# Optimization experiments

Hardware: AMD Instinct MI355X
Metric: run time of the kernel (lower is better)

The kernel has to match this reference:

```python
import jax, jax.numpy as jnp
import numpy as np

K = 32
START = K - 2  # index of <START>
STOP = K - 1   # index of <STOP>
NEG = -10000.0
B, T = 512, 2048


def setup_inputs() -> dict:
    key = jax.random.key(0)
    k1, k2, k3, k4 = jax.random.split(key, 4)
    feats = jax.random.normal(k1, (B, T, K), dtype=jnp.float32)
    transitions = jax.random.normal(k2, (K, K), dtype=jnp.float32)
    # constraints set in __init__: never transition TO START, never FROM STOP
    transitions = transitions.at[START, :].set(NEG).at[:, STOP].set(NEG)
    tags = jax.random.randint(k3, (B, T), 0, K - 2)          # real tags only
    lens = jnp.maximum(jax.random.randint(k4, (B,), 0, T), 1)  # at least 1 token
    return {"feats": feats, "transitions": transitions, "tags": tags, "lens": lens}


def _crf_loss(feats, transitions, tags, lens):
    Bn, Tn, Kn = feats.shape
    # ---- forward algorithm (log-partition) ----
    init = jnp.full((Bn, Kn), NEG, feats.dtype).at[:, START].set(0.0)

    def step(alpha, emit):
        # alpha[b,prev] + trans[next,prev] -> logsumexp over prev, then + emit[b,next]
        nxt = jax.scipy.special.logsumexp(
            alpha[:, None, :] + transitions[None, :, :], axis=2) + emit
        return nxt, nxt

    _, alphas = jax.lax.scan(step, init, jnp.swapaxes(feats, 0, 1))  # [T,B,K]
    alphas = jnp.concatenate([init[None], alphas], axis=0)           # [T+1,B,K]
    alpha_at_len = alphas[lens, jnp.arange(Bn)]                      # [B,K]
    forward_score = jax.scipy.special.logsumexp(
        alpha_at_len + transitions[STOP][None, :], axis=1)           # [B]

    # ---- gold score ----
    tags_stop = jnp.where(jnp.arange(Tn)[None, :] < lens[:, None], tags, STOP)
    pad_start = jnp.concatenate(
        [jnp.full((Bn, 1), START, tags.dtype), tags], axis=1)        # [B,T+1]
    pad_stop = jnp.concatenate(
        [tags_stop, jnp.full((Bn, 1), STOP, tags.dtype)], axis=1)    # [B,T+1]
    trans_mask = jnp.arange(Tn + 1)[None, :] <= lens[:, None]        # len+1 transitions
    trans_sc = jnp.where(trans_mask, transitions[pad_stop, pad_start], 0.0).sum(axis=1)
    emit_mask = jnp.arange(Tn)[None, :] < lens[:, None]
    emit_sc = jnp.where(
        emit_mask,
        jnp.take_along_axis(feats, tags[:, :, None], axis=2)[..., 0],
        0.0).sum(axis=1)
    gold_score = trans_sc + emit_sc

    return jnp.mean(forward_score - gold_score)


def reference(feats, transitions, tags, lens):
    return _crf_loss(feats, transitions, tags, lens)
```

## Files before the change

### kernel.cpp

```cpp
#include <hip/hip_runtime.h>
#include <cstdint>
#include <cstddef>

#define Kn 32
#define Bn 512
#define Tn 2048
#define CH 128
#define NC (Tn / CH)
#define GP 4
#define MMB (Bn * 2)
#define GB  Bn
#define START 30
#define STOP 31
#define LN2F 0.69314718055994530942f

typedef __attribute__((ext_vector_type(8))) short bf16x8;
typedef __attribute__((ext_vector_type(16))) float f32x16;
typedef __attribute__((ext_vector_type(2))) float f32x2;

union BF8 { bf16x8 v; unsigned u[4]; };

__device__ __forceinline__ unsigned pk2z(float lo, float hi) {
  return __builtin_amdgcn_perm(__float_as_uint(hi), __float_as_uint(lo),
                               0x07060302u);
}

__device__ __forceinline__ float bcast32(float v, int idx) {
  return __shfl(v, idx, 32);
}

__device__ __forceinline__ void plswap(unsigned& a, unsigned& b) {
  asm("v_permlane32_swap_b32 %0, %1" : "+v"(a), "+v"(b));
}

struct Chain {
  unsigned bu[8];
  f32x16 acc;
  float off;
  float ring[8];
  const float* fb;
  int lim;
};

__global__ __launch_bounds__(256, 3) void crf_fused(
    const float* __restrict__ feats, const float* __restrict__ trans,
    const int* __restrict__ tags, const int* __restrict__ lens,
    float* __restrict__ pmats, float* __restrict__ poffs,
    float* __restrict__ gold_part) {
  const int wid = threadIdx.x >> 6;
  const int lane = threadIdx.x & 63;

  if (blockIdx.x < MMB) {
    const int b = blockIdx.x >> 1;
    const int widx = (blockIdx.x & 1) * 4 + wid;
    const int len = lens[b];
    const int c0 = 2 * widx, c1 = c0 + 1;
    const int n0 = min(max(len - c0 * CH, 0), CH);
    const int n1 = min(max(len - c1 * CH, 0), CH);
    if (n0 == 0) return;

    const int m = lane & 31;
    const int h = lane >> 5;

    f32x2 e1[4], e2[4];
    {
      const float* tr = trans + m * Kn + 8 * h;
#pragma unroll
      for (int j = 0; j < 4; ++j) {
        e1[j] = (f32x2){__expf(tr[2 * j]) * 0.0078125f,
                        __expf(tr[2 * j + 1]) * 0.0078125f};
        e2[j] = (f32x2){__expf(tr[16 + 2 * j]) * 0.0078125f,
                        __expf(tr[16 + 2 * j + 1]) * 0.0078125f};
      }
    }
    const f32x16 zf = {0.f, 0.f, 0.f, 0.f, 0.f, 0.f, 0.f, 0.f,
                       0.f, 0.f, 0.f, 0.f, 0.f, 0.f, 0.f, 0.f};

    auto init_chain = [&](Chain& ch, int c) {
      unsigned i1[4] = {0, 0, 0, 0}, i2[4] = {0, 0, 0, 0};
      int j = m - 8 * h;
      if (0 <= j && j < 8) i1[j >> 1] = (j & 1) ? 0x3F800000u : 0x00003F80u;
      j = m - 16 - 8 * h;
      if (0 <= j && j < 8) i2[j >> 1] = (j & 1) ? 0x3F800000u : 0x00003F80u;
#pragma unroll
      for (int k = 0; k < 4; ++k) { ch.bu[k] = i1[k]; ch.bu[4 + k] = i2[k]; }
      ch.off = 0.f;
      const int t0 = c * CH;
      ch.fb = feats + ((size_t)b * Tn + t0) * Kn + m;
      ch.lim = Tn - 1 - t0;
#pragma unroll
      for (int i = 0; i < 8; ++i) ch.ring[i] = ch.fb[(size_t)min(i, ch.lim) * Kn];
    };

    auto mm = [&](Chain& ch, float f, bool rn) {
      const float w = __expf(f);
      const f32x2 w2 = {w, w};
      BF8 A1, A2, B1, B2;
#pragma unroll
      for (int j = 0; j < 4; ++j) {
        const f32x2 p1 = e1[j] * w2;
        const f32x2 p2 = e2[j] * w2;
        A1.u[j] = pk2z(p1.x, p1.y);
        A2.u[j] = pk2z(p2.x, p2.y);
        B1.u[j] = ch.bu[j];
        B2.u[j] = ch.bu[4 + j];
      }
      f32x16 acc = __builtin_amdgcn_mfma_f32_32x32x16_bf16(A2.v, B2.v, zf, 0, 0, 0);
      acc = __builtin_amdgcn_mfma_f32_32x32x16_bf16(A1.v, B1.v, acc, 0, 0, 0);

      if (rn) {
        float mx = acc[0];
#pragma unroll
        for (int r = 1; r < 16; ++r) mx = fmaxf(mx, acc[r]);
#pragma unroll
        for (int d = 1; d < 64; d <<= 1) mx = fmaxf(mx, __shfl_xor(mx, d));
        const int e = (int)((__float_as_uint(mx) >> 23) & 255u);
        const float sc = __uint_as_float((unsigned)(254 - e) << 23);
#pragma unroll
        for (int r = 0; r < 16; ++r) acc[r] *= sc;
        ch.off += (float)(e - 127) * LN2F;
      }

      unsigned qa = pk2z(acc[0], acc[1]);
      unsigned qb = pk2z(acc[2], acc[3]);
      unsigned qc = pk2z(acc[4], acc[5]);
      unsigned qd = pk2z(acc[6], acc[7]);
      unsigned qe = pk2z(acc[8], acc[9]);
      unsigned qf = pk2z(acc[10], acc[11]);
      unsigned qg = pk2z(acc[12], acc[13]);
      unsigned qh = pk2z(acc[14], acc[15]);
      plswap(qa, qc);
      plswap(qb, qd);
      plswap(qe, qg);
      plswap(qf, qh);
      ch.bu[0] = qa; ch.bu[1] = qb; ch.bu[2] = qc; ch.bu[3] = qd;
      ch.bu[4] = qe; ch.bu[5] = qf; ch.bu[6] = qg; ch.bu[7] = qh;
      ch.acc = acc;
    };

    Chain ch0, ch1;
    init_chain(ch0, c0);
    if (n1) init_chain(ch1, c1);

    const int nb0 = n0 >> 3;
    const int nb1 = n1 >> 3;
    int t = 0;
    for (int mb = 0; mb < nb1; ++mb) {
#pragma unroll
      for (int i = 0; i < 8; ++i) {
        const float f0 = ch0.ring[i];
        ch0.ring[i] = ch0.fb[(size_t)min(t + i + 8, ch0.lim) * Kn];
        const float f1 = ch1.ring[i];
        ch1.ring[i] = ch1.fb[(size_t)min(t + i + 8, ch1.lim) * Kn];
        const bool rn = ((t + i) & 31) == 31;
        mm(ch0, f0, rn);
        mm(ch1, f1, rn);
      }
      t += 8;
    }
    for (int mb = nb1; mb < nb0; ++mb) {
#pragma unroll
      for (int i = 0; i < 8; ++i) {
        const float f0 = ch0.ring[i];
        ch0.ring[i] = ch0.fb[(size_t)min(t + i + 8, ch0.lim) * Kn];
        mm(ch0, f0, ((t + i) & 31) == 31);
      }
      t += 8;
    }
    const int r0 = n0 & 7;
    for (int i = 0; i < r0; ++i) mm(ch0, ch0.ring[i], false);
    const int r1 = n1 & 7;
    for (int i = 0; i < r1; ++i) mm(ch1, ch1.ring[i], false);

    {
      float* pm = pmats + (size_t)(b * NC + c0) * (Kn * Kn);
#pragma unroll
      for (int r = 0; r < 16; ++r) {
        const int row = (r & 3) + 8 * (r >> 2) + 4 * h;
        pm[row * Kn + m] = ch0.acc[r];
      }
      if (lane == 0) poffs[b * NC + c0] = ch0.off + 7.0f * LN2F * (float)n0;
    }
    if (n1) {
      float* pm = pmats + (size_t)(b * NC + c1) * (Kn * Kn);
#pragma unroll
      for (int r = 0; r < 16; ++r) {
        const int row = (r & 3) + 8 * (r >> 2) + 4 * h;
        pm[row * Kn + m] = ch1.acc[r];
      }
      if (lane == 0) poffs[b * NC + c1] = ch1.off + 7.0f * LN2F * (float)n1;
    }
  } else {
    const int b = blockIdx.x - MMB;
    const int len = lens[b];
    const int* tg = tags + (size_t)b * Tn;
    const float* fbp = feats + (size_t)b * Tn * Kn;
    float acc = 0.f;
    for (int tt = 64 * wid + lane; tt < len; tt += 256) {
      const int tag = tg[tt];
      const int prev = tt ? tg[tt - 1] : START;
      acc += fbp[(size_t)tt * Kn + tag] + trans[tag * Kn + prev];
      if (tt == len - 1) acc += trans[STOP * Kn + tag];
    }
#pragma unroll
    for (int msk = 32; msk >= 1; msk >>= 1) acc += __shfl_xor(acc, msk);
    if (lane == 0) gold_part[b * GP + wid] = acc;
  }
}

__device__ __forceinline__ float renorm_s(float& s, float off) {
  int e = (int)((__float_as_uint(s) >> 23) & 255u);
  e = max(e, __shfl_xor(e, 1));
  e = max(e, __shfl_xor(e, 2));
  e = max(e, __shfl_xor(e, 4));
  e = max(e, __shfl_xor(e, 8));
  e = max(e, __shfl_xor(e, 16));
  s *= __uint_as_float((unsigned)(254 - e) << 23);
  return off + (float)(e - 127) * LN2F;
}

__global__ __launch_bounds__(256, 2) void crf_apply(
    const float* __restrict__ trans, const int* __restrict__ lens,
    const float* __restrict__ pmats, const float* __restrict__ poffs,
    const float* __restrict__ gold_part, float* __restrict__ out) {
  __shared__ float4 smat[NC * 256];
  const int tid = threadIdx.x;
  const int b = blockIdx.x;
  const int len = lens[b];
  const int nc = (len + CH - 1) / CH;

  const float4* gp = (const float4*)(pmats + (size_t)b * NC * (Kn * Kn));
  for (int qq = tid; qq < nc * 256; qq += 256) {
    const int row = (qq >> 3) & 31;
    const int g = qq & 7;
    smat[(qq & ~7) | (g ^ (row & 7))] = gp[qq];
  }
  __syncthreads();
  if (tid >= 64) return;

  const int lane = tid;
  const int n = lane & 31;
  const int hb = (lane >> 5) * 16;
  const int g0 = hb >> 2;
  const int nsw = n & 7;
  float s = (n == START) ? 1.0f : 0.0f;
  float off = 0.0f;
  for (int c = 0; c < nc; ++c) {
    const float4* mr = &smat[(c << 8) | (n << 3)];
    const float4 p0 = mr[(g0 + 0) ^ nsw];
    const float4 p1 = mr[(g0 + 1) ^ nsw];
    const float4 p2 = mr[(g0 + 2) ^ nsw];
    const float4 p3 = mr[(g0 + 3) ^ nsw];
    float a0 = 0.f, a1 = 0.f, a2 = 0.f, a3 = 0.f;
    a0 = fmaf(bcast32(s, hb + 0), p0.x, a0);
    a0 = fmaf(bcast32(s, hb + 1), p0.y, a0);
    a0 = fmaf(bcast32(s, hb + 2), p0.z, a0);
    a0 = fmaf(bcast32(s, hb + 3), p0.w, a0);
    a1 = fmaf(bcast32(s, hb + 4), p1.x, a1);
    a1 = fmaf(bcast32(s, hb + 5), p1.y, a1);
    a1 = fmaf(bcast32(s, hb + 6), p1.z, a1);
    a1 = fmaf(bcast32(s, hb + 7), p1.w, a1);
    a2 = fmaf(bcast32(s, hb + 8), p2.x, a2);
    a2 = fmaf(bcast32(s, hb + 9), p2.y, a2);
    a2 = fmaf(bcast32(s, hb + 10), p2.z, a2);
    a2 = fmaf(bcast32(s, hb + 11), p2.w, a2);
    a3 = fmaf(bcast32(s, hb + 12), p3.x, a3);
    a3 = fmaf(bcast32(s, hb + 13), p3.y, a3);
    a3 = fmaf(bcast32(s, hb + 14), p3.z, a3);
    a3 = fmaf(bcast32(s, hb + 15), p3.w, a3);
    float p = (a0 + a1) + (a2 + a3);
    p += __shfl_xor(p, 32);
    s = p;
    off = renorm_s(s, off);
    off += poffs[b * NC + c];
  }
  const float es = __expf(trans[STOP * Kn + n]);
  float q = s * es;
#pragma unroll
  for (int d = 1; d < 32; d <<= 1) q += __shfl_xor(q, d);
  if (lane == 0) {
    const float fs = __logf(q) + off;
    float gs = 0.f;
#pragma unroll
    for (int gi = 0; gi < GP; ++gi) gs += gold_part[b * GP + gi];
    atomicAdd(out, (fs - gs) * (1.0f / (float)Bn));
  }
}

extern "C" void kernel_launch(void* const* d_in, const int* in_sizes, int n_in,
                              void* d_out, int out_size, void* d_ws, size_t ws_size,
                              hipStream_t stream) {
  const float* feats = (const float*)d_in[0];
  const float* trans = (const float*)d_in[1];
  const int* tags = (const int*)d_in[2];
  const int* lens = (const int*)d_in[3];

  float* gold_part = (float*)d_ws;
  float* poffs = gold_part + (size_t)Bn * GP;
  float* pmats = poffs + (size_t)Bn * NC;

  hipMemsetAsync(d_out, 0, (size_t)out_size * sizeof(float), stream);
  crf_fused<<<MMB + GB, 256, 0, stream>>>(feats, trans, tags, lens, pmats,
                                          poffs, gold_part);
  crf_apply<<<Bn, 256, 0, stream>>>(trans, lens, pmats, poffs, gold_part,
                                    (float*)d_out);
}
```

Before: 286.0 us.

## Use one chunk per wave with LDS double-buffered feature staging

Each wave now processes a single 128-step chunk instead of interleaving two independent chains, and the grid grows from two to four blocks per batch row. Feature rows are loaded from global memory as coalesced float4 loads into a per-wave double-buffered LDS staging area 32 timesteps deep, replacing strided scalar global loads. The next quarter is prefetched while the current one is computed. Occupancy hint rises from 3 to 4 blocks per CU. Dropping the second chain removes the instruction-level parallelism that hid MFMA latency across two dependent recurrences, which may expose the serial dependency chain.

```diff
diff --git a/kernel.cpp b/kernel.cpp
--- a/kernel.cpp
+++ b/kernel.cpp
@@ -8,11 +8,13 @@
 #define CH 128
 #define NC (Tn / CH)
 #define GP 4
-#define MMB (Bn * 2)
+#define MMB (Bn * (NC / 4))
 #define GB  Bn
 #define START 30
 #define STOP 31
 #define LN2F 0.69314718055994530942f
+#define QS 32
+#define QF (QS * Kn)
 
 typedef __attribute__((ext_vector_type(8))) short bf16x8;
 typedef __attribute__((ext_vector_type(16))) float f32x16;
@@ -33,31 +35,21 @@
   asm("v_permlane32_swap_b32 %0, %1" : "+v"(a), "+v"(b));
 }
 
-struct Chain {
-  unsigned bu[8];
-  f32x16 acc;
-  float off;
-  float ring[8];
-  const float* fb;
-  int lim;
-};
-
-__global__ __launch_bounds__(256, 3) void crf_fused(
+__global__ __launch_bounds__(256, 4) void crf_fused(
     const float* __restrict__ feats, const float* __restrict__ trans,
     const int* __restrict__ tags, const int* __restrict__ lens,
     float* __restrict__ pmats, float* __restrict__ poffs,
     float* __restrict__ gold_part) {
+  __shared__ float lds[4][2][QF];
   const int wid = threadIdx.x >> 6;
   const int lane = threadIdx.x & 63;
 
   if (blockIdx.x < MMB) {
-    const int b = blockIdx.x >> 1;
-    const int widx = (blockIdx.x & 1) * 4 + wid;
+    const int b = blockIdx.x >> 2;
+    const int c = (blockIdx.x & 3) * 4 + wid;
     const int len = lens[b];
-    const int c0 = 2 * widx, c1 = c0 + 1;
-    const int n0 = min(max(len - c0 * CH, 0), CH);
-    const int n1 = min(max(len - c1 * CH, 0), CH);
-    if (n0 == 0) return;
+    const int nsteps = min(max(len - c * CH, 0), CH);
+    if (nsteps == 0) return;
 
     const int m = lane & 31;
     const int h = lane >> 5;
@@ -73,26 +65,24 @@
                         __expf(tr[16 + 2 * j + 1]) * 0.0078125f};
       }
     }
+    unsigned bu[8];
+    {
+      const int j1 = m - 8 * h;
+      const int j2 = m - 16 - 8 * h;
+#pragma unroll
+      for (int k = 0; k < 4; ++k) {
+        bu[k] = (j1 == 2 * k) ? 0x00003F80u
+                              : (j1 == 2 * k + 1) ? 0x3F800000u : 0u;
+        bu[4 + k] = (j2 == 2 * k) ? 0x00003F80u
+                                  : (j2 == 2 * k + 1) ? 0x3F800000u : 0u;
+      }
+    }
     const f32x16 zf = {0.f, 0.f, 0.f, 0.f, 0.f, 0.f, 0.f, 0.f,
                        0.f, 0.f, 0.f, 0.f, 0.f, 0.f, 0.f, 0.f};
-
-    auto init_chain = [&](Chain& ch, int c) {
-      unsigned i1[4] = {0, 0, 0, 0}, i2[4] = {0, 0, 0, 0};
-      int j = m - 8 * h;
-      if (0 <= j && j < 8) i1[j >> 1] = (j & 1) ? 0x3F800000u : 0x00003F80u;
-      j = m - 16 - 8 * h;
-      if (0 <= j && j < 8) i2[j >> 1] = (j & 1) ? 0x3F800000u : 0x00003F80u;
-#pragma unroll
-      for (int k = 0; k < 4; ++k) { ch.bu[k] = i1[k]; ch.bu[4 + k] = i2[k]; }
-      ch.off = 0.f;
-      const int t0 = c * CH;
-      ch.fb = feats + ((size_t)b * Tn + t0) * Kn + m;
-      ch.lim = Tn - 1 - t0;
-#pragma unroll
-      for (int i = 0; i < 8; ++i) ch.ring[i] = ch.fb[(size_t)min(i, ch.lim) * Kn];
-    };
-
-    auto mm = [&](Chain& ch, float f, bool rn) {
+    f32x16 acc;
+    float off = 0.0f;
+
+    auto mmstep = [&](float f, bool rn) {
       const float w = __expf(f);
       const f32x2 w2 = {w, w};
       BF8 A1, A2, B1, B2;
@@ -102,10 +92,10 @@
         const f32x2 p2 = e2[j] * w2;
         A1.u[j] = pk2z(p1.x, p1.y);
         A2.u[j] = pk2z(p2.x, p2.y);
-        B1.u[j] = ch.bu[j];
-        B2.u[j] = ch.bu[4 + j];
-      }
-      f32x16 acc = __builtin_amdgcn_mfma_f32_32x32x16_bf16(A2.v, B2.v, zf, 0, 0, 0);
+        B1.u[j] = bu[j];
+        B2.u[j] = bu[4 + j];
+      }
+      acc = __builtin_amdgcn_mfma_f32_32x32x16_bf16(A2.v, B2.v, zf, 0, 0, 0);
       acc = __builtin_amdgcn_mfma_f32_32x32x16_bf16(A1.v, B1.v, acc, 0, 0, 0);
 
       if (rn) {
@@ -118,7 +108,7 @@
         const float sc = __uint_as_float((unsigned)(254 - e) << 23);
 #pragma unroll
         for (int r = 0; r < 16; ++r) acc[r] *= sc;
-        ch.off += (float)(e - 127) * LN2F;
+        off += (float)(e - 127) * LN2F;
       }
 
       unsigned qa = pk2z(acc[0], acc[1]);
@@ -133,63 +123,74 @@
       plswap(qb, qd);
       plswap(qe, qg);
       plswap(qf, qh);
-      ch.bu[0] = qa; ch.bu[1] = qb; ch.bu[2] = qc; ch.bu[3] = qd;
-      ch.bu[4] = qe; ch.bu[5] = qf; ch.bu[6] = qg; ch.bu[7] = qh;
-      ch.acc = acc;
+      bu[0] = qa; bu[1] = qb; bu[2] = qc; bu[3] = qd;
+      bu[4] = qe; bu[5] = qf; bu[6] = qg; bu[7] = qh;
     };
 
-    Chain ch0, ch1;
-    init_chain(ch0, c0);
-    if (n1) init_chain(ch1, c1);
-
-    const int nb0 = n0 >> 3;
-    const int nb1 = n1 >> 3;
-    int t = 0;
-    for (int mb = 0; mb < nb1; ++mb) {
-#pragma unroll
-      for (int i = 0; i < 8; ++i) {
-        const float f0 = ch0.ring[i];
-        ch0.ring[i] = ch0.fb[(size_t)min(t + i + 8, ch0.lim) * Kn];
-        const float f1 = ch1.ring[i];
-        ch1.ring[i] = ch1.fb[(size_t)min(t + i + 8, ch1.lim) * Kn];
-        const bool rn = ((t + i) & 31) == 31;
-        mm(ch0, f0, rn);
-        mm(ch1, f1, rn);
-      }
-      t += 8;
-    }
-    for (int mb = nb1; mb < nb0; ++mb) {
-#pragma unroll
-      for (int i = 0; i < 8; ++i) {
-        const float f0 = ch0.ring[i];
-        ch0.ring[i] = ch0.fb[(size_t)min(t + i + 8, ch0.lim) * Kn];
-        mm(ch0, f0, ((t + i) & 31) == 31);
-      }
-      t += 8;
-    }
-    const int r0 = n0 & 7;
-    for (int i = 0; i < r0; ++i) mm(ch0, ch0.ring[i], false);
-    const int r1 = n1 & 7;
-    for (int i = 0; i < r1; ++i) mm(ch1, ch1.ring[i], false);
+    const float* gsrc = feats + ((size_t)b * Tn + (size_t)c * CH) * Kn;
+    float* myl = &lds[wid][0][0];
 
     {
-      float* pm = pmats + (size_t)(b * NC + c0) * (Kn * Kn);
-#pragma unroll
-      for (int r = 0; r < 16; ++r) {
-        const int row = (r & 3) + 8 * (r >> 2) + 4 * h;
-        pm[row * Kn + m] = ch0.acc[r];
-      }
-      if (lane == 0) poffs[b * NC + c0] = ch0.off + 7.0f * LN2F * (float)n0;
-    }
-    if (n1) {
-      float* pm = pmats + (size_t)(b * NC + c1) * (Kn * Kn);
-#pragma unroll
-      for (int r = 0; r < 16; ++r) {
-        const int row = (r & 3) + 8 * (r >> 2) + 4 * h;
-        pm[row * Kn + m] = ch1.acc[r];
-      }
-      if (lane == 0) poffs[b * NC + c1] = ch1.off + 7.0f * LN2F * (float)n1;
-    }
+      float4 v0 = *(const float4*)(gsrc + 0 * 256 + lane * 4);
+      float4 v1 = *(const float4*)(gsrc + 1 * 256 + lane * 4);
+      float4 v2 = *(const float4*)(gsrc + 2 * 256 + lane * 4);
+      float4 v3 = *(const float4*)(gsrc + 3 * 256 + lane * 4);
+      *(float4*)(myl + 0 * 256 + lane * 4) = v0;
+      *(float4*)(myl + 1 * 256 + lane * 4) = v1;
+      *(float4*)(myl + 2 * 256 + lane * 4) = v2;
+      *(float4*)(myl + 3 * 256 + lane * 4) = v3;
+    }
+
+    const int nq = (nsteps + QS - 1) / QS;
+    for (int q = 0; q < nq; ++q) {
+      float4 nv0, nv1, nv2, nv3;
+      const bool more = (q + 1 < nq);
+      if (more) {
+        const float* g = gsrc + (q + 1) * QF + lane * 4;
+        nv0 = *(const float4*)(g + 0 * 256);
+        nv1 = *(const float4*)(g + 1 * 256);
+        nv2 = *(const float4*)(g + 2 * 256);
+        nv3 = *(const float4*)(g + 3 * 256);
+      }
+
+      const float* lbuf = myl + (q & 1) * QF;
+      const int ns = min(QS, nsteps - q * QS);
+      float fr[8];
+#pragma unroll
+      for (int i = 0; i < 8; ++i) fr[i] = lbuf[i * Kn + m];
+
+      const int nb = ns >> 3;
+      int tq = 0;
+      for (int s8 = 0; s8 < nb; ++s8) {
+#pragma unroll
+        for (int i = 0; i < 8; ++i) {
+          const float f = fr[i];
+          fr[i] = lbuf[min(tq + i + 8, QS - 1) * Kn + m];
+          mmstep(f, (tq + i) == 31);
+        }
+        tq += 8;
+      }
+      const int rem = ns & 7;
+#pragma unroll
+      for (int i = 0; i < 8; ++i)
+        if (i < rem) mmstep(fr[i], false);
+
+      if (more) {
+        float* nbuf = myl + ((q + 1) & 1) * QF;
+        *(float4*)(nbuf + 0 * 256 + lane * 4) = nv0;
+        *(float4*)(nbuf + 1 * 256 + lane * 4) = nv1;
+        *(float4*)(nbuf + 2 * 256 + lane * 4) = nv2;
+        *(float4*)(nbuf + 3 * 256 + lane * 4) = nv3;
+      }
+    }
+
+    float* pm = pmats + (size_t)(b * NC + c) * (Kn * Kn);
+#pragma unroll
+    for (int r = 0; r < 16; ++r) {
+      const int row = (r & 3) + 8 * (r >> 2) + 4 * h;
+      pm[row * Kn + m] = acc[r];
+    }
+    if (lane == 0) poffs[b * NC + c] = off + 7.0f * LN2F * (float)nsteps;
   } else {
     const int b = blockIdx.x - MMB;
     const int len = lens[b];
```

New measurement: 265.5 us. -7.2%, faster.
